# Optimization experiments

Hardware: AMD Instinct MI355X
Metric: run time of the kernel (lower is better)

## Reference

```python
import jax, jax.numpy as jnp
import numpy as np

EMBED = 1024
HEADS = 16
HEAD_DIM = EMBED // HEADS
NEG = -1e20


def setup_inputs() -> dict:
    key = jax.random.key(0)
    ks = jax.random.split(key, 8)
    N, S = 2, 2048
    values = jax.random.normal(ks[0], (N, S, EMBED), dtype=jnp.float32)
    keys = jax.random.normal(ks[1], (N, S, EMBED), dtype=jnp.float32)
    queries = jax.random.normal(ks[2], (N, S, EMBED), dtype=jnp.float32)
    mask = jnp.ones((N, 1, 1, S), dtype=jnp.int32)
    s = 1.0 / np.sqrt(HEAD_DIM)
    Wv = jax.random.normal(ks[3], (HEAD_DIM, HEAD_DIM), dtype=jnp.float32) * s
    Wk = jax.random.normal(ks[4], (HEAD_DIM, HEAD_DIM), dtype=jnp.float32) * s
    Wq = jax.random.normal(ks[5], (HEAD_DIM, HEAD_DIM), dtype=jnp.float32) * s
    Wo = jax.random.normal(ks[6], (EMBED, EMBED), dtype=jnp.float32) * (1.0 / np.sqrt(EMBED))
    bo = jnp.zeros((EMBED,), dtype=jnp.float32)
    return {"values": values, "keys": keys, "queries": queries, "mask": mask,
            "Wv": Wv, "Wk": Wk, "Wq": Wq, "Wo": Wo, "bo": bo}


def reference(values, keys, queries, mask, Wv, Wk, Wq, Wo, bo):
    N, q_len, E = queries.shape
    v_len, k_len = values.shape[1], keys.shape[1]
    H, D = HEADS, HEAD_DIM
    # split heads: [N, L, H, D]
    v = values.reshape(N, v_len, H, D)
    k = keys.reshape(N, k_len, H, D)
    q = queries.reshape(N, q_len, H, D)
    # per-head linear projections (shared across heads), torch Linear: x @ W.T
    v = jnp.einsum('nlhd,ed->nlhe', v, Wv)
    k = jnp.einsum('nlhd,ed->nlhe', k, Wk)
    q = jnp.einsum('nlhd,ed->nlhe', q, Wq)
    # scores [N, H, q, k]
    scores = jnp.einsum('nqhd,nkhd->nhqk', q, k)
    scores = jnp.where(mask == 0, NEG, scores)
    # NOTE: original scales by sqrt(embed_size), not sqrt(head_dim)
    attn = jax.nn.softmax(scores / (E ** 0.5), axis=3)
    out = jnp.einsum('nhqk,nkhd->nqhd', attn, v).reshape(N, q_len, E)
    return out @ Wo.T + bo
```

## Files before the change

### kernel.cpp

```cpp
#include <hip/hip_runtime.h>

typedef __bf16 bf16_t;
typedef __bf16 bf16x8 __attribute__((ext_vector_type(8)));
typedef __bf16 bf16x4 __attribute__((ext_vector_type(4)));
typedef float f32x4 __attribute__((ext_vector_type(4)));
typedef float f32x16 __attribute__((ext_vector_type(16)));

#define MFMA16(a, b, c) __builtin_amdgcn_mfma_f32_16x16x32_bf16((a), (b), (c), 0, 0, 0)
#define MFMA32(a, b, c) __builtin_amdgcn_mfma_f32_32x32x16_bf16((a), (b), (c), 0, 0, 0)

namespace {
constexpr int S_LEN = 2048;
constexpr int EMB   = 1024;
constexpr int HEADS = 16;
constexpr int HD    = 64;
constexpr float Q_PRESCALE = 1.44269504088896340736f / 32.0f;
constexpr float NEG_L2     = -4.5084e18f;
}

__device__ __forceinline__ bf16x8 load8_cvt(const float* __restrict__ p) {
    const f32x4 a = *(const f32x4*)p;
    const f32x4 b = *(const f32x4*)(p + 4);
    bf16x8 r;
    r[0] = (bf16_t)a[0]; r[1] = (bf16_t)a[1]; r[2] = (bf16_t)a[2]; r[3] = (bf16_t)a[3];
    r[4] = (bf16_t)b[0]; r[5] = (bf16_t)b[1]; r[6] = (bf16_t)b[2]; r[7] = (bf16_t)b[3];
    return r;
}

__device__ __forceinline__ unsigned pk_bf16(float lo, float hi) {
    union { bf16_t h[2]; unsigned u; } u;
    u.h[0] = (bf16_t)lo; u.h[1] = (bf16_t)hi;
    return u.u;
}

__global__ __launch_bounds__(256) void proj_kernel(
    const float* __restrict__ values, const float* __restrict__ keys,
    const float* __restrict__ queries,
    const float* __restrict__ Wv, const float* __restrict__ Wk,
    const float* __restrict__ Wq,
    bf16_t* __restrict__ Qp, bf16_t* __restrict__ Kf, bf16_t* __restrict__ Vf)
{
    const int tid = threadIdx.x;
    const int w = tid >> 6, l = tid & 63, g = l >> 4, q15 = l & 15;
    const int b   = blockIdx.x;
    const int mat = b >> 10;
    const int rem = b & 1023;
    const int h   = rem >> 6;
    const int t0  = (((rem & 63) << 2) + w) << 4;
    const int n   = t0 >> 11;
    const int s0  = t0 & 2047;

    if (mat < 2) {
        const float* X = (mat == 0) ? queries : keys;
        const float* W = (mat == 0) ? Wq : Wk;
        const float scl = (mat == 0) ? Q_PRESCALE : 1.0f;
        const float* xr = X + (size_t)(t0 + q15) * EMB + h * HD + g * 8;
        bf16x8 a0 = load8_cvt(xr);
        bf16x8 a1 = load8_cvt(xr + 32);
        f32x4 acc[4];
        #pragma unroll
        for (int nt = 0; nt < 4; ++nt) acc[nt] = (f32x4){0.f, 0.f, 0.f, 0.f};
        #pragma unroll
        for (int nt = 0; nt < 4; ++nt) {
            const float* wr = W + (nt * 16 + q15) * HD + g * 8;
            bf16x8 b0 = load8_cvt(wr);
            bf16x8 b1 = load8_cvt(wr + 32);
            acc[nt] = MFMA16(a0, b0, acc[nt]);
            acc[nt] = MFMA16(a1, b1, acc[nt]);
        }
        if (mat == 0) {
            bf16_t* O = Qp + (size_t)(n * HEADS + h) * S_LEN * HD;
            #pragma unroll
            for (int nt = 0; nt < 4; ++nt)
                #pragma unroll
                for (int r = 0; r < 4; ++r)
                    O[(size_t)(s0 + g * 4 + r) * HD + nt * 16 + q15] = (bf16_t)(acc[nt][r] * scl);
        } else {
            bf16_t* O = Kf + (size_t)(n * HEADS + h) * S_LEN * HD;
            const int ktb  = s0 >> 5;
            const int lrow = s0 & 31;
            const int hi8  = (q15 >> 3) * 256 + (q15 & 7);
            #pragma unroll
            for (int nt = 0; nt < 4; ++nt)
                #pragma unroll
                for (int r = 0; r < 4; ++r)
                    O[(size_t)(ktb * 4 + nt) * 512 + hi8 + (lrow + g * 4 + r) * 8]
                        = (bf16_t)acc[nt][r];
        }
    } else {
        const float* xr = values + (size_t)(t0 + q15) * EMB + h * HD + g * 8;
        bf16x8 b0 = load8_cvt(xr);
        bf16x8 b1 = load8_cvt(xr + 32);
        bf16_t* O = Vf + (size_t)(n * HEADS + h) * S_LEN * HD;
        f32x4 acc[4];
        #pragma unroll
        for (int et = 0; et < 4; ++et) acc[et] = (f32x4){0.f, 0.f, 0.f, 0.f};
        #pragma unroll
        for (int et = 0; et < 4; ++et) {
            const float* wr = Wv + (et * 16 + q15) * HD + g * 8;
            bf16x8 a0 = load8_cvt(wr);
            bf16x8 a1 = load8_cvt(wr + 32);
            acc[et] = MFMA16(a0, b0, acc[et]);
            acc[et] = MFMA16(a1, b1, acc[et]);
        }
        const int kt2 = (s0 >> 6) * 2;
        const int ksl = (s0 >> 4) & 3;
        const int hi8 = (q15 >> 3) * 256 + (q15 & 7);
        #pragma unroll
        for (int et = 0; et < 4; ++et)
            #pragma unroll
            for (int r = 0; r < 4; ++r)
                O[(size_t)((kt2 + (et >> 1)) * 4 + ksl) * 512 + hi8
                  + ((et & 1) * 16 + g * 4 + r) * 8] = (bf16_t)acc[et][r];
    }
}

__global__ __launch_bounds__(256, 2) void attn_kernel(
    const bf16_t* __restrict__ Qp, const bf16_t* __restrict__ Kf,
    const bf16_t* __restrict__ Vf, const int* __restrict__ mask,
    bf16_t* __restrict__ AO)
{
    __shared__ bf16_t plds[4][32][72];
    const int tid = threadIdx.x;
    const int w = tid >> 6, l = tid & 63;
    const int l31 = l & 31, hi = l >> 5;
    const int bid = blockIdx.x;
    const int nh = bid & 31, qt = bid >> 5;
    const int n = nh >> 4, h = nh & 15;
    const size_t hb = (size_t)nh * S_LEN * HD;
    const int qb = qt * 128 + w * 32;

    bf16x8 qf[4];
    {
        const bf16_t* qr = Qp + hb + (size_t)(qb + l31) * HD + hi * 8;
        #pragma unroll
        for (int d = 0; d < 4; ++d) qf[d] = *(const bf16x8*)(qr + d * 16);
    }

    const int* __restrict__ mrow = mask + n * S_LEN;
    const bf16_t* kp0 = Kf + hb + (size_t)l * 8;
    const bf16_t* vp0 = Vf + hb + (size_t)l * 8;

    bool anyZero = false;
    {
        const int* mp = mrow + (l >> 1) * 64 + (l & 1) * 32;
        #pragma unroll
        for (int j = 0; j < 8; ++j) {
            const int4 mv = *(const int4*)(mp + 4 * j);
            anyZero |= (mv.x == 0) | (mv.y == 0) | (mv.z == 0) | (mv.w == 0);
        }
    }
    const unsigned long long maskbal = __ballot(anyZero);

    f32x16 acc0, acc1;
    #pragma unroll
    for (int i = 0; i < 16; ++i) { acc0[i] = 0.f; acc1[i] = 0.f; }
    float l_run = 0.0f;

    bf16x8 kbuf0[8], kbuf1[8];
    auto loadK = [&](bf16x8* buf, int kt_) {
        const bf16_t* p = kp0 + (size_t)(kt_ * 8) * 512;
        #pragma unroll
        for (int j = 0; j < 8; ++j) buf[j] = *(const bf16x8*)(p + j * 512);
    };

    auto tile = [&](int kt, bf16x8* kf, bf16x8* nkf, bool pref) {
        bf16x8 vf[8];
        {
            const bf16_t* p = vp0 + (size_t)(kt * 8) * 512;
            #pragma unroll
            for (int j = 0; j < 8; ++j) vf[j] = *(const bf16x8*)(p + j * 512);
        }

        f32x16 s0, s1;
        #pragma unroll
        for (int i = 0; i < 16; ++i) { s0[i] = 0.f; s1[i] = 0.f; }
        #pragma unroll
        for (int d = 0; d < 4; ++d) s0 = MFMA32(kf[d],     qf[d], s0);
        #pragma unroll
        for (int d = 0; d < 4; ++d) s1 = MFMA32(kf[4 + d], qf[d], s1);

        if (pref) loadK(nkf, kt + 1);

        if ((maskbal >> (2 * kt)) & 3ull) {
            const unsigned long long mb = __ballot(mrow[kt * 64 + l] != 0);
            #pragma unroll
            for (int r = 0; r < 16; ++r) {
                const int cr = (r & 3) + 8 * (r >> 2) + 4 * hi;
                if (!((mb >> cr) & 1ull))        s0[r] = NEG_L2;
                if (!((mb >> (32 + cr)) & 1ull)) s1[r] = NEG_L2;
            }
        }

        float ts0 = 0.f, ts1 = 0.f;
        #pragma unroll
        for (int r = 0; r < 16; ++r) {
            const float p0 = exp2f(s0[r]);
            const float p1 = exp2f(s1[r]);
            s0[r] = p0; s1[r] = p1;
            ts0 += p0; ts1 += p1;
        }
        l_run += ts0 + ts1;

        union U8 { unsigned u[4]; bf16x8 v; };
        bf16x8 pa[4];
        #pragma unroll
        for (int b = 0; b < 2; ++b) {
            #pragma unroll
            for (int t = 0; t < 2; ++t) {
                const int rb = t * 8;
                float e0, e1, e2, e3, e4, e5, e6, e7;
                if (b == 0) {
                    e0 = s0[rb]; e1 = s0[rb + 1]; e2 = s0[rb + 2]; e3 = s0[rb + 3];
                    e4 = s0[rb + 4]; e5 = s0[rb + 5]; e6 = s0[rb + 6]; e7 = s0[rb + 7];
                } else {
                    e0 = s1[rb]; e1 = s1[rb + 1]; e2 = s1[rb + 2]; e3 = s1[rb + 3];
                    e4 = s1[rb + 4]; e5 = s1[rb + 5]; e6 = s1[rb + 6]; e7 = s1[rb + 7];
                }
                const unsigned a01 = pk_bf16(e0, e1);
                const unsigned a23 = pk_bf16(e2, e3);
                const unsigned b01 = pk_bf16(e4, e5);
                const unsigned b23 = pk_bf16(e6, e7);
                const unsigned y1 = hi ? a01 : b01;
                const unsigned y2 = hi ? a23 : b23;
                const unsigned r1 = (unsigned)__shfl_xor((int)y1, 32);
                const unsigned r2 = (unsigned)__shfl_xor((int)y2, 32);
                U8 f;
                f.u[0] = hi ? r1 : a01;
                f.u[1] = hi ? r2 : a23;
                f.u[2] = hi ? b01 : r1;
                f.u[3] = hi ? b23 : r2;
                pa[2 * b + t] = f.v;
            }
        }

        #pragma unroll
        for (int ksl = 0; ksl < 4; ++ksl) {
            acc0 = MFMA32(pa[ksl], vf[ksl],     acc0);
            acc1 = MFMA32(pa[ksl], vf[4 + ksl], acc1);
        }
    };

    loadK(kbuf0, 0);
    for (int kt = 0; kt < 32; kt += 2) {
        tile(kt,     kbuf0, kbuf1, true);
        tile(kt + 1, kbuf1, kbuf0, kt + 1 < 31);
    }

    const float l_tot = l_run + __shfl_xor(l_run, 32);
    const float inv = 1.0f / l_tot;
    #pragma unroll
    for (int r = 0; r < 16; ++r) {
        const int cr = (r & 3) + 8 * (r >> 2) + 4 * hi;
        const float iq = __shfl(inv, cr);
        plds[w][cr][l31]      = (bf16_t)(acc0[r] * iq);
        plds[w][cr][32 + l31] = (bf16_t)(acc1[r] * iq);
    }
    __syncthreads();

    const int rr = l >> 1, c0 = (l & 1) * 32;
    const bf16x8 o0 = *(const bf16x8*)&plds[w][rr][c0];
    const bf16x8 o1 = *(const bf16x8*)&plds[w][rr][c0 + 8];
    const bf16x8 o2 = *(const bf16x8*)&plds[w][rr][c0 + 16];
    const bf16x8 o3 = *(const bf16x8*)&plds[w][rr][c0 + 24];
    bf16_t* op = AO + (size_t)(n * S_LEN + qb + rr) * EMB + h * HD + c0;
    *(bf16x8*)(op)      = o0;
    *(bf16x8*)(op + 8)  = o1;
    *(bf16x8*)(op + 16) = o2;
    *(bf16x8*)(op + 24) = o3;
}

__global__ __launch_bounds__(256) void outproj_kernel(
    const bf16_t* __restrict__ X, const float* __restrict__ Wo,
    const float* __restrict__ bo, float* __restrict__ out)
{
    __shared__ bf16_t Xs[128 * 64];
    __shared__ bf16_t Ws[64 * 64];
    const int tid = threadIdx.x;
    const int w = tid >> 6, l = tid & 63, g = l >> 4, q15 = l & 15;
    const int m0 = (blockIdx.x >> 4) * 128;
    const int n0 = (blockIdx.x & 15) * 64;
    const int wm = (w >> 1) * 64, wn = (w & 1) * 32;

    f32x4 acc[4][2];
    #pragma unroll
    for (int i = 0; i < 4; ++i)
        #pragma unroll
        for (int j = 0; j < 2; ++j) acc[i][j] = (f32x4){0.f, 0.f, 0.f, 0.f};

    for (int k0 = 0; k0 < EMB; k0 += 64) {
        __syncthreads();
        #pragma unroll
        for (int j = 0; j < 4; ++j) {
            const int cid = tid + 256 * j;
            const int r = cid >> 3, pc = cid & 7;
            const int sw = (pc ^ (r & 7)) * 8;
            *(bf16x8*)&Xs[r * 64 + sw] =
                *(const bf16x8*)(X + (size_t)(m0 + r) * EMB + k0 + pc * 8);
        }
        #pragma unroll
        for (int j = 0; j < 2; ++j) {
            const int cid = tid + 256 * j;
            const int r = cid >> 3, pc = cid & 7;
            const int sw = (pc ^ (r & 7)) * 8;
            *(bf16x8*)&Ws[r * 64 + sw] =
                load8_cvt(Wo + (size_t)(n0 + r) * EMB + k0 + pc * 8);
        }
        __syncthreads();
        #pragma unroll
        for (int c = 0; c < 2; ++c) {
            bf16x8 av[4], bv[2];
            #pragma unroll
            for (int mt = 0; mt < 4; ++mt) {
                const int r = wm + mt * 16 + q15;
                av[mt] = *(const bf16x8*)&Xs[r * 64 + (((4 * c + g) ^ (r & 7)) * 8)];
            }
            #pragma unroll
            for (int nt = 0; nt < 2; ++nt) {
                const int r = wn + nt * 16 + q15;
                bv[nt] = *(const bf16x8*)&Ws[r * 64 + (((4 * c + g) ^ (r & 7)) * 8)];
            }
            #pragma unroll
            for (int mt = 0; mt < 4; ++mt)
                #pragma unroll
                for (int nt = 0; nt < 2; ++nt)
                    acc[mt][nt] = MFMA16(av[mt], bv[nt], acc[mt][nt]);
        }
    }

    float bias[2];
    #pragma unroll
    for (int nt = 0; nt < 2; ++nt) bias[nt] = bo[n0 + wn + nt * 16 + q15];
    #pragma unroll
    for (int mt = 0; mt < 4; ++mt)
        #pragma unroll
        for (int nt = 0; nt < 2; ++nt)
            #pragma unroll
            for (int r = 0; r < 4; ++r)
                out[(size_t)(m0 + wm + mt * 16 + g * 4 + r) * EMB + n0 + wn + nt * 16 + q15]
                    = acc[mt][nt][r] + bias[nt];
}

extern "C" void kernel_launch(void* const* d_in, const int* in_sizes, int n_in,
                              void* d_out, int out_size, void* d_ws, size_t ws_size,
                              hipStream_t stream) {
    const float* values  = (const float*)d_in[0];
    const float* keys    = (const float*)d_in[1];
    const float* queries = (const float*)d_in[2];
    const int*   mask    = (const int*)d_in[3];
    const float* Wv      = (const float*)d_in[4];
    const float* Wk      = (const float*)d_in[5];
    const float* Wq      = (const float*)d_in[6];
    const float* Wo      = (const float*)d_in[7];
    const float* bo      = (const float*)d_in[8];
    float* out = (float*)d_out;

    bf16_t* Qp = (bf16_t*)d_ws;
    bf16_t* Kf = Qp + (size_t)4194304;
    bf16_t* Vf = Kf + (size_t)4194304;
    bf16_t* AO = Vf + (size_t)4194304;

    proj_kernel<<<3072, 256, 0, stream>>>(values, keys, queries, Wv, Wk, Wq, Qp, Kf, Vf);
    attn_kernel<<<512, 256, 0, stream>>>(Qp, Kf, Vf, mask, AO);
    outproj_kernel<<<512, 256, 0, stream>>>(AO, Wo, bo, out);
}
```

Before: 124.2 us.

## Split attention over the key dimension into two halves and merge the partial outputs

```diff
diff --git a/kernel.cpp b/kernel.cpp
--- a/kernel.cpp
+++ b/kernel.cpp
@@ -115,20 +115,25 @@
     }
 }
 
+template<int SPLIT>
 __global__ __launch_bounds__(256, 2) void attn_kernel(
     const bf16_t* __restrict__ Qp, const bf16_t* __restrict__ Kf,
     const bf16_t* __restrict__ Vf, const int* __restrict__ mask,
-    bf16_t* __restrict__ AO)
+    bf16_t* __restrict__ Out, float* __restrict__ Lp)
 {
     __shared__ bf16_t plds[4][32][72];
     const int tid = threadIdx.x;
     const int w = tid >> 6, l = tid & 63;
     const int l31 = l & 31, hi = l >> 5;
     const int bid = blockIdx.x;
-    const int nh = bid & 31, qt = bid >> 5;
+    const int half = (SPLIT == 2) ? (bid >> 9) : 0;
+    const int rem  = bid & 511;
+    const int nh = rem & 31, qt = rem >> 5;
     const int n = nh >> 4, h = nh & 15;
     const size_t hb = (size_t)nh * S_LEN * HD;
     const int qb = qt * 128 + w * 32;
+    const int kt0 = half * (32 / SPLIT);
+    const int ktN = kt0 + 32 / SPLIT;
 
     bf16x8 qf[4];
     {
@@ -241,33 +246,79 @@
         }
     };
 
-    loadK(kbuf0, 0);
-    for (int kt = 0; kt < 32; kt += 2) {
+    loadK(kbuf0, kt0);
+    for (int kt = kt0; kt < ktN; kt += 2) {
         tile(kt,     kbuf0, kbuf1, true);
-        tile(kt + 1, kbuf1, kbuf0, kt + 1 < 31);
+        tile(kt + 1, kbuf1, kbuf0, kt + 1 < ktN - 1);
     }
 
     const float l_tot = l_run + __shfl_xor(l_run, 32);
-    const float inv = 1.0f / l_tot;
+    if (SPLIT == 1) {
+        const float inv = 1.0f / l_tot;
+        #pragma unroll
+        for (int r = 0; r < 16; ++r) {
+            const int cr = (r & 3) + 8 * (r >> 2) + 4 * hi;
+            const float iq = __shfl(inv, cr);
+            plds[w][cr][l31]      = (bf16_t)(acc0[r] * iq);
+            plds[w][cr][32 + l31] = (bf16_t)(acc1[r] * iq);
+        }
+        __syncthreads();
+        const int rr = l >> 1, c0 = (l & 1) * 32;
+        const bf16x8 o0 = *(const bf16x8*)&plds[w][rr][c0];
+        const bf16x8 o1 = *(const bf16x8*)&plds[w][rr][c0 + 8];
+        const bf16x8 o2 = *(const bf16x8*)&plds[w][rr][c0 + 16];
+        const bf16x8 o3 = *(const bf16x8*)&plds[w][rr][c0 + 24];
+        bf16_t* op = Out + (size_t)(n * S_LEN + qb + rr) * EMB + h * HD + c0;
+        *(bf16x8*)(op)      = o0;
+        *(bf16x8*)(op + 8)  = o1;
+        *(bf16x8*)(op + 16) = o2;
+        *(bf16x8*)(op + 24) = o3;
+    } else {
+        #pragma unroll
+        for (int r = 0; r < 16; ++r) {
+            const int cr = (r & 3) + 8 * (r >> 2) + 4 * hi;
+            plds[w][cr][l31]      = (bf16_t)acc0[r];
+            plds[w][cr][32 + l31] = (bf16_t)acc1[r];
+        }
+        if (hi == 0) Lp[(half << 16) + nh * S_LEN + qb + l31] = l_tot;
+        __syncthreads();
+        const int rr = l >> 1, c0 = (l & 1) * 32;
+        const bf16x8 o0 = *(const bf16x8*)&plds[w][rr][c0];
+        const bf16x8 o1 = *(const bf16x8*)&plds[w][rr][c0 + 8];
+        const bf16x8 o2 = *(const bf16x8*)&plds[w][rr][c0 + 16];
+        const bf16x8 o3 = *(const bf16x8*)&plds[w][rr][c0 + 24];
+        bf16_t* op = Out + ((size_t)(half * 32 + nh) * S_LEN + qb + rr) * HD + c0;
+        *(bf16x8*)(op)      = o0;
+        *(bf16x8*)(op + 8)  = o1;
+        *(bf16x8*)(op + 16) = o2;
+        *(bf16x8*)(op + 24) = o3;
+    }
+}
+
+__global__ __launch_bounds__(256) void merge_kernel(
+    const bf16_t* __restrict__ Opart, const float* __restrict__ Lp,
+    bf16_t* __restrict__ AO)
+{
+    const int gid = blockIdx.x * 256 + threadIdx.x;
+    const int gq = gid >> 2, seg = (gid & 3) * 16;
+    const int nh = gq >> 11, s = gq & 2047;
+    const int n = nh >> 4, h = nh & 15;
+    const float inv = 1.0f / (Lp[gq] + Lp[65536 + gq]);
+    const bf16_t* p0 = Opart + (size_t)gq * HD + seg;
+    const bf16_t* p1 = p0 + (size_t)32 * S_LEN * HD;
+    const bf16x8 a0 = *(const bf16x8*)(p0);
+    const bf16x8 a1 = *(const bf16x8*)(p0 + 8);
+    const bf16x8 b0 = *(const bf16x8*)(p1);
+    const bf16x8 b1 = *(const bf16x8*)(p1 + 8);
+    bf16x8 r0, r1;
     #pragma unroll
-    for (int r = 0; r < 16; ++r) {
-        const int cr = (r & 3) + 8 * (r >> 2) + 4 * hi;
-        const float iq = __shfl(inv, cr);
-        plds[w][cr][l31]      = (bf16_t)(acc0[r] * iq);
-        plds[w][cr][32 + l31] = (bf16_t)(acc1[r] * iq);
-    }
-    __syncthreads();
-
-    const int rr = l >> 1, c0 = (l & 1) * 32;
-    const bf16x8 o0 = *(const bf16x8*)&plds[w][rr][c0];
-    const bf16x8 o1 = *(const bf16x8*)&plds[w][rr][c0 + 8];
-    const bf16x8 o2 = *(const bf16x8*)&plds[w][rr][c0 + 16];
-    const bf16x8 o3 = *(const bf16x8*)&plds[w][rr][c0 + 24];
-    bf16_t* op = AO + (size_t)(n * S_LEN + qb + rr) * EMB + h * HD + c0;
-    *(bf16x8*)(op)      = o0;
-    *(bf16x8*)(op + 8)  = o1;
-    *(bf16x8*)(op + 16) = o2;
-    *(bf16x8*)(op + 24) = o3;
+    for (int j = 0; j < 8; ++j) {
+        r0[j] = (bf16_t)(((float)a0[j] + (float)b0[j]) * inv);
+        r1[j] = (bf16_t)(((float)a1[j] + (float)b1[j]) * inv);
+    }
+    bf16_t* op = AO + (size_t)(n * S_LEN + s) * EMB + h * HD + seg;
+    *(bf16x8*)(op)     = r0;
+    *(bf16x8*)(op + 8) = r1;
 }
 
 __global__ __launch_bounds__(256) void outproj_kernel(
@@ -355,12 +406,22 @@
     const float* bo      = (const float*)d_in[8];
     float* out = (float*)d_out;
 
-    bf16_t* Qp = (bf16_t*)d_ws;
-    bf16_t* Kf = Qp + (size_t)4194304;
-    bf16_t* Vf = Kf + (size_t)4194304;
-    bf16_t* AO = Vf + (size_t)4194304;
+    bf16_t* Qp    = (bf16_t*)d_ws;
+    bf16_t* Kf    = Qp + (size_t)4194304;
+    bf16_t* Vf    = Kf + (size_t)4194304;
+    bf16_t* AO    = Vf + (size_t)4194304;
+    bf16_t* Opart = AO + (size_t)4194304;
+    float*  Lp    = (float*)((char*)d_ws + (size_t)48 * 1024 * 1024);
 
     proj_kernel<<<3072, 256, 0, stream>>>(values, keys, queries, Wv, Wk, Wq, Qp, Kf, Vf);
-    attn_kernel<<<512, 256, 0, stream>>>(Qp, Kf, Vf, mask, AO);
+
+    const bool split2 = ws_size >= (size_t)50 * 1024 * 1024;
+    if (split2) {
+        attn_kernel<2><<<1024, 256, 0, stream>>>(Qp, Kf, Vf, mask, Opart, Lp);
+        merge_kernel<<<1024, 256, 0, stream>>>(Opart, Lp, AO);
+    } else {
+        attn_kernel<1><<<512, 256, 0, stream>>>(Qp, Kf, Vf, mask, AO, nullptr);
+    }
+
     outproj_kernel<<<512, 256, 0, stream>>>(AO, Wo, bo, out);
 }
```

New measurement: 129.7 us. 1.04x slower.
